# Performance work log

Measured on AMD Instinct MI355X. Metric: run time of the kernel, lower is better.

## Reference

```python
import jax, jax.numpy as jnp
import numpy as np


def _base_index(H, W, dtype=jnp.float32):
    # Homogeneous pixel coordinates (x, y, 1) per pixel, shape [H, W, 3].
    x = jnp.arange(W, dtype=dtype)
    y = jnp.arange(H, dtype=dtype)
    xx, yy = jnp.meshgrid(x, y)  # [H, W]
    return jnp.stack([xx, yy, jnp.ones_like(xx)], axis=-1)


def _bilinear_resample(image, coords):
    # image: [B, H, W, C]; coords: [B, H, W, 2] in (x, y) order (tf resampler convention).
    # Out-of-bounds corners contribute zero (zero padding), matching tfa.image.resampler.
    B, H, W, C = image.shape
    x = coords[..., 0]
    y = coords[..., 1]
    x0 = jnp.floor(x)
    y0 = jnp.floor(y)
    wx1 = x - x0
    wy1 = y - y0
    wx0 = 1.0 - wx1
    wy0 = 1.0 - wy1
    x0i = x0.astype(jnp.int32)
    y0i = y0.astype(jnp.int32)
    x1i = x0i + 1
    y1i = y0i + 1

    def corner(yi, xi, w):
        valid = (xi >= 0) & (xi < W) & (yi >= 0) & (yi < H)
        xc = jnp.clip(xi, 0, W - 1)
        yc = jnp.clip(yi, 0, H - 1)
        # gather per batch: [B, H, W, C]
        g = jax.vmap(lambda im, yy, xx: im[yy, xx])(image, yc, xc)
        return g * (w * valid.astype(image.dtype))[..., None]

    return (corner(y0i, x0i, wy0 * wx0) + corner(y0i, x1i, wy0 * wx1)
            + corner(y1i, x0i, wy1 * wx0) + corner(y1i, x1i, wy1 * wx1))


def setup_inputs() -> dict:
    key = jax.random.key(0)
    k1, k2, k3 = jax.random.split(key, 3)
    B, H, W, C = 4, 512, 640, 16
    image_tensor = jax.random.normal(k1, (B, H, W, C), dtype=jnp.float32)
    # positive depths around 1
    depth_tensor = 0.5 + jax.random.uniform(k2, (B, H, W), dtype=jnp.float32)
    # near-identity projective transform so sampled coords land mostly in-bounds
    eye = jnp.eye(4, dtype=jnp.float32)[None].repeat(B, axis=0)
    project_tensor = eye + 0.001 * jax.random.normal(k3, (B, 4, 4), dtype=jnp.float32)
    return {"image_tensor": image_tensor, "depth_tensor": depth_tensor,
            "project_tensor": project_tensor}


def reference(image_tensor, depth_tensor, project_tensor):
    B, H, W, C = image_tensor.shape
    base = _base_index(H, W, image_tensor.dtype)  # [H, W, 3]
    R = project_tensor[:, :3, :3]                 # [B, 3, 3]
    t = project_tensor[:, :3, 3]                  # [B, 3]
    # tf.tensordot(R, base, [-1,-1]) -> [B,3,H,W]; transpose -> [B,H,W,3]
    rotate = jnp.einsum('bij,hwj->bhwi', R, base)
    sample = rotate * depth_tensor[..., None] + t[:, None, None, :]  # [B,H,W,3]
    coords = sample[..., :2] / sample[..., 2:3]                       # [B,H,W,2] (x,y)
    return _bilinear_resample(image_tensor, coords)
```

## Files before the change

kernel.cpp:

```cpp
#include <hip/hip_runtime.h>

constexpr int B  = 4;
constexpr int H  = 512;
constexpr int Wd = 640;
constexpr int NPIX_IMG = H * Wd;
constexpr int BLOCK = 256;
constexpr int PIX_PER_BLOCK  = BLOCK / 4;
constexpr int BLOCKS_PER_ROW = Wd / PIX_PER_BLOCK;
constexpr int BLOCKS_PER_IMG = H * BLOCKS_PER_ROW;
constexpr int GRID = B * BLOCKS_PER_IMG;
static_assert(Wd % PIX_PER_BLOCK == 0, "block must tile a row exactly");
static_assert(GRID * BLOCK == B * NPIX_IMG * 4, "prefetch exactly covers image");

typedef float f32x4 __attribute__((ext_vector_type(4)));

__global__ __launch_bounds__(256) void depth_project_kernel(
    const float* __restrict__ image,
    const float* __restrict__ depth,
    const float* __restrict__ proj,
    float4* __restrict__ out)
{
    const int blk = blockIdx.x;
    const int tix = threadIdx.x;

    const f32x4* img_v = (const f32x4*)image;
    f32x4 pf = img_v[blk * BLOCK + tix];

    const int b   = blk / BLOCKS_PER_IMG;
    const int rem = blk % BLOCKS_PER_IMG;
    const int h   = rem / BLOCKS_PER_ROW;
    const int wb  = (rem % BLOCKS_PER_ROW) * PIX_PER_BLOCK;

    const int c4  = tix & 3;
    const int pl  = tix >> 2;
    const int w   = wb + pl;
    const int pix = (b * H + h) * Wd + w;

    const float* P = proj + b * 16;
    const float x = (float)w;
    const float y = (float)h;
    const float d = depth[pix];

    float sx = (P[0] * x + P[1] * y + P[2])  * d + P[3];
    float sy = (P[4] * x + P[5] * y + P[6])  * d + P[7];
    float sz = (P[8] * x + P[9] * y + P[10]) * d + P[11];
    float cx = sx / sz;
    float cy = sy / sz;

    float x0f = floorf(cx), y0f = floorf(cy);
    float wx1 = cx - x0f,   wy1 = cy - y0f;
    float wx0 = 1.0f - wx1, wy0 = 1.0f - wy1;
    int x0 = (int)x0f, y0 = (int)y0f;
    int x1 = x0 + 1,   y1 = y0 + 1;

    float vx0 = (x0 >= 0 && x0 < Wd) ? 1.0f : 0.0f;
    float vx1 = (x1 >= 0 && x1 < Wd) ? 1.0f : 0.0f;
    float vy0 = (y0 >= 0 && y0 < H)  ? 1.0f : 0.0f;
    float vy1 = (y1 >= 0 && y1 < H)  ? 1.0f : 0.0f;

    int x0c = min(max(x0, 0), Wd - 1);
    int x1c = min(max(x1, 0), Wd - 1);
    int y0c = min(max(y0, 0), H - 1);
    int y1c = min(max(y1, 0), H - 1);

    float w00 = wy0 * wx0 * vy0 * vx0;
    float w01 = wy0 * wx1 * vy0 * vx1;
    float w10 = wy1 * wx0 * vy1 * vx0;
    float w11 = wy1 * wx1 * vy1 * vx1;

    asm volatile("" :: "v"(pf.x), "v"(pf.y), "v"(pf.z), "v"(pf.w));

    const float4* img4 = (const float4*)image;
    const int base_b = b * (NPIX_IMG * 4);
    float4 g00 = img4[base_b + (y0c * Wd + x0c) * 4 + c4];
    float4 g01 = img4[base_b + (y0c * Wd + x1c) * 4 + c4];
    float4 g10 = img4[base_b + (y1c * Wd + x0c) * 4 + c4];
    float4 g11 = img4[base_b + (y1c * Wd + x1c) * 4 + c4];

    f32x4 r;
    r.x = g00.x * w00 + g01.x * w01 + g10.x * w10 + g11.x * w11;
    r.y = g00.y * w00 + g01.y * w01 + g10.y * w10 + g11.y * w11;
    r.z = g00.z * w00 + g01.z * w01 + g10.z * w10 + g11.z * w11;
    r.w = g00.w * w00 + g01.w * w01 + g10.w * w10 + g11.w * w11;

    f32x4* out_v = (f32x4*)out;
    __builtin_nontemporal_store(r, out_v + pix * 4 + c4);
}

extern "C" void kernel_launch(void* const* d_in, const int* in_sizes, int n_in,
                              void* d_out, int out_size, void* d_ws, size_t ws_size,
                              hipStream_t stream) {
    const float* image = (const float*)d_in[0];
    const float* depth = (const float*)d_in[1];
    const float* proj  = (const float*)d_in[2];
    float4* out = (float4*)d_out;

    depth_project_kernel<<<GRID, BLOCK, 0, stream>>>(image, depth, proj, out);
}
```

Baseline: 155.0 us.

## Stage two source rows in shared memory and gather bilinear corners from LDS

Each block now covers 128 pixels and cooperatively loads a two-row, 144-column window of the source image into a swizzled shared-memory tile. The window is placed using the projected coordinate of the block's middle pixel. Bilinear corners are read from LDS when they fall inside the window and from global memory otherwise. This removes the old whole-image prefetch trick and the redundant global gathers, and depth is now read with a nontemporal load. In exchange it adds two barriers and a serial dependency before any gather can start, and relies on the transform being near identity for the window to hit.

```diff
diff --git a/kernel.cpp b/kernel.cpp
--- a/kernel.cpp
+++ b/kernel.cpp
@@ -4,33 +4,32 @@
 constexpr int H  = 512;
 constexpr int Wd = 640;
 constexpr int NPIX_IMG = H * Wd;
-constexpr int BLOCK = 256;
-constexpr int PIX_PER_BLOCK  = BLOCK / 4;
-constexpr int BLOCKS_PER_ROW = Wd / PIX_PER_BLOCK;
-constexpr int BLOCKS_PER_IMG = H * BLOCKS_PER_ROW;
-constexpr int GRID = B * BLOCKS_PER_IMG;
-static_assert(Wd % PIX_PER_BLOCK == 0, "block must tile a row exactly");
-static_assert(GRID * BLOCK == B * NPIX_IMG * 4, "prefetch exactly covers image");
+constexpr int PXB   = 128;
+constexpr int BLOCK = PXB * 4;
+constexpr int BPR   = Wd / PXB;
+constexpr int GRID  = B * H * BPR;
+constexpr int SW    = 144;
+constexpr int XMARG = PXB / 2 + 7;
+static_assert(Wd % PXB == 0, "block tiles a row exactly");
 
 typedef float f32x4 __attribute__((ext_vector_type(4)));
 
-__global__ __launch_bounds__(256) void depth_project_kernel(
+__global__ __launch_bounds__(BLOCK, 8) void depth_project_kernel(
     const float* __restrict__ image,
     const float* __restrict__ depth,
     const float* __restrict__ proj,
     float4* __restrict__ out)
 {
+    __shared__ float4 tile[2][SW][4];
+    __shared__ int cons[2];
+
     const int blk = blockIdx.x;
+    const int b   = blk / (H * BPR);
+    const int rem = blk % (H * BPR);
+    const int h   = rem / BPR;
+    const int wb  = (rem % BPR) * PXB;
+
     const int tix = threadIdx.x;
-
-    const f32x4* img_v = (const f32x4*)image;
-    f32x4 pf = img_v[blk * BLOCK + tix];
-
-    const int b   = blk / BLOCKS_PER_IMG;
-    const int rem = blk % BLOCKS_PER_IMG;
-    const int h   = rem / BLOCKS_PER_ROW;
-    const int wb  = (rem % BLOCKS_PER_ROW) * PIX_PER_BLOCK;
-
     const int c4  = tix & 3;
     const int pl  = tix >> 2;
     const int w   = wb + pl;
@@ -39,7 +38,7 @@
     const float* P = proj + b * 16;
     const float x = (float)w;
     const float y = (float)h;
-    const float d = depth[pix];
+    const float d = __builtin_nontemporal_load(depth + pix);
 
     float sx = (P[0] * x + P[1] * y + P[2])  * d + P[3];
     float sy = (P[4] * x + P[5] * y + P[6])  * d + P[7];
@@ -52,6 +51,29 @@
     float wx0 = 1.0f - wx1, wy0 = 1.0f - wy1;
     int x0 = (int)x0f, y0 = (int)y0f;
     int x1 = x0 + 1,   y1 = y0 + 1;
+
+    if (tix == BLOCK / 2) {
+        cons[0] = min(max(y0, -8), H + 8);
+        cons[1] = min(max(x0 - XMARG, -2 * SW), Wd + SW);
+    }
+    __syncthreads();
+    const int yhat = cons[0];
+    const int xlo  = cons[1];
+    const int rid0 = min(max(yhat,     0), H - 1);
+    const int rid1 = min(max(yhat + 1, 0), H - 1);
+
+    const float4* img4 = (const float4*)image;
+    const int ibase = b * (NPIX_IMG * 4);
+    for (int e = tix; e < 2 * SW * 4; e += BLOCK) {
+        int r   = (e >= SW * 4) ? 1 : 0;
+        int rm  = e - r * (SW * 4);
+        int col = rm >> 2;
+        int c   = rm & 3;
+        int xc  = min(max(xlo + col, 0), Wd - 1);
+        int rid = r ? rid1 : rid0;
+        tile[r][col][c ^ ((col >> 1) & 3)] = img4[ibase + (rid * Wd + xc) * 4 + c];
+    }
+    __syncthreads();
 
     float vx0 = (x0 >= 0 && x0 < Wd) ? 1.0f : 0.0f;
     float vx1 = (x1 >= 0 && x1 < Wd) ? 1.0f : 0.0f;
@@ -68,14 +90,35 @@
     float w10 = wy1 * wx0 * vy1 * vx0;
     float w11 = wy1 * wx1 * vy1 * vx1;
 
-    asm volatile("" :: "v"(pf.x), "v"(pf.y), "v"(pf.z), "v"(pf.w));
+    const int j0 = x0c - xlo, j1 = x1c - xlo;
+    const bool jok0 = (unsigned)j0 < (unsigned)SW;
+    const bool jok1 = (unsigned)j1 < (unsigned)SW;
+    const int rs0 = (y0c == rid0) ? 0 : ((y0c == rid1) ? 1 : -1);
+    const int rs1 = (y1c == rid0) ? 0 : ((y1c == rid1) ? 1 : -1);
+    const bool h00 = jok0 && (rs0 >= 0);
+    const bool h01 = jok1 && (rs0 >= 0);
+    const bool h10 = jok0 && (rs1 >= 0);
+    const bool h11 = jok1 && (rs1 >= 0);
 
-    const float4* img4 = (const float4*)image;
-    const int base_b = b * (NPIX_IMG * 4);
-    float4 g00 = img4[base_b + (y0c * Wd + x0c) * 4 + c4];
-    float4 g01 = img4[base_b + (y0c * Wd + x1c) * 4 + c4];
-    float4 g10 = img4[base_b + (y1c * Wd + x0c) * 4 + c4];
-    float4 g11 = img4[base_b + (y1c * Wd + x1c) * 4 + c4];
+    const int j0s = min(max(j0, 0), SW - 1);
+    const int j1s = min(max(j1, 0), SW - 1);
+    const int r0s = max(rs0, 0);
+    const int r1s = max(rs1, 0);
+    const int sl0 = c4 ^ ((j0s >> 1) & 3);
+    const int sl1 = c4 ^ ((j1s >> 1) & 3);
+
+    float4 g00 = tile[r0s][j0s][sl0];
+    float4 g01 = tile[r0s][j1s][sl1];
+    float4 g10 = tile[r1s][j0s][sl0];
+    float4 g11 = tile[r1s][j1s][sl1];
+
+    if (!(h00 && h01 && h10 && h11)) {
+        const float4* ib = img4 + ibase;
+        if (!h00) g00 = ib[(y0c * Wd + x0c) * 4 + c4];
+        if (!h01) g01 = ib[(y0c * Wd + x1c) * 4 + c4];
+        if (!h10) g10 = ib[(y1c * Wd + x0c) * 4 + c4];
+        if (!h11) g11 = ib[(y1c * Wd + x1c) * 4 + c4];
+    }
 
     f32x4 r;
     r.x = g00.x * w00 + g01.x * w01 + g10.x * w10 + g11.x * w11;
```

After: 169.0 us. 1.09x slower.

## Process full image rows per block with software-pipelined prefetch and XCD swizzle

Applied to the files above, without the earlier changes.

Each block now handles one whole image row in 64-pixel chunks instead of a single chunk, so the grid shrinks to one block per row. A block index swizzle places consecutive rows on the same XCD so neighbouring gathers can share L2. Depth and an image-prefetch vector for the next chunk are loaded while the current chunk's gathers run. This cuts launch and per-block overhead and improves cache locality, but reduces the number of waves in flight and serialises work inside each block.

```diff
diff --git a/kernel.cpp b/kernel.cpp
--- a/kernel.cpp
+++ b/kernel.cpp
@@ -5,12 +5,12 @@
 constexpr int Wd = 640;
 constexpr int NPIX_IMG = H * Wd;
 constexpr int BLOCK = 256;
-constexpr int PIX_PER_BLOCK  = BLOCK / 4;
-constexpr int BLOCKS_PER_ROW = Wd / PIX_PER_BLOCK;
-constexpr int BLOCKS_PER_IMG = H * BLOCKS_PER_ROW;
-constexpr int GRID = B * BLOCKS_PER_IMG;
-static_assert(Wd % PIX_PER_BLOCK == 0, "block must tile a row exactly");
-static_assert(GRID * BLOCK == B * NPIX_IMG * 4, "prefetch exactly covers image");
+constexpr int ROWS  = B * H;
+constexpr int GRID  = ROWS;
+constexpr int CHUNK = 64;
+constexpr int NCH   = Wd / CHUNK;
+static_assert(NCH * CHUNK == Wd, "chunks tile the row exactly");
+static_assert(ROWS % 8 == 0, "XCD swizzle needs rows % 8 == 0");
 
 typedef float f32x4 __attribute__((ext_vector_type(4)));
 
@@ -23,68 +23,77 @@
     const int blk = blockIdx.x;
     const int tix = threadIdx.x;
 
-    const f32x4* img_v = (const f32x4*)image;
-    f32x4 pf = img_v[blk * BLOCK + tix];
+    const int row = (blk & 7) * (ROWS / 8) + (blk >> 3);
+    const int b   = row / H;
+    const int h   = row % H;
 
-    const int b   = blk / BLOCKS_PER_IMG;
-    const int rem = blk % BLOCKS_PER_IMG;
-    const int h   = rem / BLOCKS_PER_ROW;
-    const int wb  = (rem % BLOCKS_PER_ROW) * PIX_PER_BLOCK;
-
-    const int c4  = tix & 3;
-    const int pl  = tix >> 2;
-    const int w   = wb + pl;
-    const int pix = (b * H + h) * Wd + w;
+    const int c4 = tix & 3;
+    const int pl = tix >> 2;
+    const int rowpix = row * Wd;
 
     const float* P = proj + b * 16;
-    const float x = (float)w;
     const float y = (float)h;
-    const float d = depth[pix];
 
-    float sx = (P[0] * x + P[1] * y + P[2])  * d + P[3];
-    float sy = (P[4] * x + P[5] * y + P[6])  * d + P[7];
-    float sz = (P[8] * x + P[9] * y + P[10]) * d + P[11];
-    float cx = sx / sz;
-    float cy = sy / sz;
+    const f32x4*  img_v = (const f32x4*)image;
+    const float4* img4  = (const float4*)image;
+    const int ibase = b * (NPIX_IMG * 4);
+    f32x4* out_v = (f32x4*)out;
 
-    float x0f = floorf(cx), y0f = floorf(cy);
-    float wx1 = cx - x0f,   wy1 = cy - y0f;
-    float wx0 = 1.0f - wx1, wy0 = 1.0f - wy1;
-    int x0 = (int)x0f, y0 = (int)y0f;
-    int x1 = x0 + 1,   y1 = y0 + 1;
+    float d_cur = depth[rowpix + pl];
+    f32x4 pf = img_v[rowpix * 4 + tix];
 
-    float vx0 = (x0 >= 0 && x0 < Wd) ? 1.0f : 0.0f;
-    float vx1 = (x1 >= 0 && x1 < Wd) ? 1.0f : 0.0f;
-    float vy0 = (y0 >= 0 && y0 < H)  ? 1.0f : 0.0f;
-    float vy1 = (y1 >= 0 && y1 < H)  ? 1.0f : 0.0f;
+    for (int n = 0; n < NCH; ++n) {
+        const int px = n * CHUNK + pl;
+        const float x = (float)px;
 
-    int x0c = min(max(x0, 0), Wd - 1);
-    int x1c = min(max(x1, 0), Wd - 1);
-    int y0c = min(max(y0, 0), H - 1);
-    int y1c = min(max(y1, 0), H - 1);
+        asm volatile("" :: "v"(pf.x), "v"(pf.y), "v"(pf.z), "v"(pf.w));
 
-    float w00 = wy0 * wx0 * vy0 * vx0;
-    float w01 = wy0 * wx1 * vy0 * vx1;
-    float w10 = wy1 * wx0 * vy1 * vx0;
-    float w11 = wy1 * wx1 * vy1 * vx1;
+        float sx = (P[0] * x + P[1] * y + P[2])  * d_cur + P[3];
+        float sy = (P[4] * x + P[5] * y + P[6])  * d_cur + P[7];
+        float sz = (P[8] * x + P[9] * y + P[10]) * d_cur + P[11];
+        float cx = sx / sz;
+        float cy = sy / sz;
 
-    asm volatile("" :: "v"(pf.x), "v"(pf.y), "v"(pf.z), "v"(pf.w));
+        float x0f = floorf(cx), y0f = floorf(cy);
+        float wx1 = cx - x0f,   wy1 = cy - y0f;
+        float wx0 = 1.0f - wx1, wy0 = 1.0f - wy1;
+        int x0 = (int)x0f, y0 = (int)y0f;
+        int x1 = x0 + 1,   y1 = y0 + 1;
 
-    const float4* img4 = (const float4*)image;
-    const int base_b = b * (NPIX_IMG * 4);
-    float4 g00 = img4[base_b + (y0c * Wd + x0c) * 4 + c4];
-    float4 g01 = img4[base_b + (y0c * Wd + x1c) * 4 + c4];
-    float4 g10 = img4[base_b + (y1c * Wd + x0c) * 4 + c4];
-    float4 g11 = img4[base_b + (y1c * Wd + x1c) * 4 + c4];
+        float vx0 = (x0 >= 0 && x0 < Wd) ? 1.0f : 0.0f;
+        float vx1 = (x1 >= 0 && x1 < Wd) ? 1.0f : 0.0f;
+        float vy0 = (y0 >= 0 && y0 < H)  ? 1.0f : 0.0f;
+        float vy1 = (y1 >= 0 && y1 < H)  ? 1.0f : 0.0f;
 
-    f32x4 r;
-    r.x = g00.x * w00 + g01.x * w01 + g10.x * w10 + g11.x * w11;
-    r.y = g00.y * w00 + g01.y * w01 + g10.y * w10 + g11.y * w11;
-    r.z = g00.z * w00 + g01.z * w01 + g10.z * w10 + g11.z * w11;
-    r.w = g00.w * w00 + g01.w * w01 + g10.w * w10 + g11.w * w11;
+        int x0c = min(max(x0, 0), Wd - 1);
+        int x1c = min(max(x1, 0), Wd - 1);
+        int y0c = min(max(y0, 0), H - 1);
+        int y1c = min(max(y1, 0), H - 1);
 
-    f32x4* out_v = (f32x4*)out;
-    __builtin_nontemporal_store(r, out_v + pix * 4 + c4);
+        float w00 = wy0 * wx0 * vy0 * vx0;
+        float w01 = wy0 * wx1 * vy0 * vx1;
+        float w10 = wy1 * wx0 * vy1 * vx0;
+        float w11 = wy1 * wx1 * vy1 * vx1;
+
+        float4 g00 = img4[ibase + (y0c * Wd + x0c) * 4 + c4];
+        float4 g01 = img4[ibase + (y0c * Wd + x1c) * 4 + c4];
+        float4 g10 = img4[ibase + (y1c * Wd + x0c) * 4 + c4];
+        float4 g11 = img4[ibase + (y1c * Wd + x1c) * 4 + c4];
+
+        const int nn = (n + 1 < NCH) ? n + 1 : NCH - 1;
+        pf = img_v[(rowpix + nn * CHUNK) * 4 + tix];
+        float d_next = depth[rowpix + nn * CHUNK + pl];
+
+        f32x4 r;
+        r.x = g00.x * w00 + g01.x * w01 + g10.x * w10 + g11.x * w11;
+        r.y = g00.y * w00 + g01.y * w01 + g10.y * w10 + g11.y * w11;
+        r.z = g00.z * w00 + g01.z * w01 + g10.z * w10 + g11.z * w11;
+        r.w = g00.w * w00 + g01.w * w01 + g10.w * w10 + g11.w * w11;
+
+        __builtin_nontemporal_store(r, out_v + (rowpix + px) * 4 + c4);
+
+        d_cur = d_next;
+    }
 }
 
 extern "C" void kernel_launch(void* const* d_in, const int* in_sizes, int n_in,
```

Result: slower. 167.4 us (+8.0%).

## Stage predicted source rows in an LDS ring buffer for bilinear gathers

Applied to the files above, without the earlier changes.

Each block now processes a 128-pixel strip over 16 output rows. It predicts which source rows the projected coordinates will hit and keeps a 4-row ring of image data with a 32-column margin in shared memory. Gathers read from LDS and fall back to global memory when a sample lands outside the staged window. Upcoming rows are prefetched into registers while the current row is computed. This aims to turn scattered global gathers into coalesced row loads that are reused across pixels. In exchange it adds two barriers per step, far less parallelism (about 1/32 as many blocks), and the removal of the old whole-image prefetch trick.

```diff
diff --git a/kernel.cpp b/kernel.cpp
--- a/kernel.cpp
+++ b/kernel.cpp
@@ -4,13 +4,17 @@
 constexpr int H  = 512;
 constexpr int Wd = 640;
 constexpr int NPIX_IMG = H * Wd;
-constexpr int BLOCK = 256;
-constexpr int PIX_PER_BLOCK  = BLOCK / 4;
-constexpr int BLOCKS_PER_ROW = Wd / PIX_PER_BLOCK;
-constexpr int BLOCKS_PER_IMG = H * BLOCKS_PER_ROW;
-constexpr int GRID = B * BLOCKS_PER_IMG;
-static_assert(Wd % PIX_PER_BLOCK == 0, "block must tile a row exactly");
-static_assert(GRID * BLOCK == B * NPIX_IMG * 4, "prefetch exactly covers image");
+constexpr int BLOCK  = 256;
+constexpr int STRIP  = 128;
+constexpr int NSTEP  = 16;
+constexpr int STRIPS = Wd / STRIP;
+constexpr int LAYERS = H / NSTEP;
+constexpr int GRID   = B * LAYERS * STRIPS;
+constexpr int XM     = 32;
+constexpr int SW     = 192;
+constexpr int SEGF4  = SW * 4;
+constexpr int RING   = 4;
+static_assert(STRIPS * STRIP == Wd && LAYERS * NSTEP == H, "exact tiling");
 
 typedef float f32x4 __attribute__((ext_vector_type(4)));
 
@@ -20,71 +24,148 @@
     const float* __restrict__ proj,
     float4* __restrict__ out)
 {
-    const int blk = blockIdx.x;
+    __shared__ f32x4 tile[RING * SEGF4];
+
+    const int blk   = blockIdx.x;
+    const int b     = blk / (LAYERS * STRIPS);
+    const int r2    = blk % (LAYERS * STRIPS);
+    const int layer = r2 / STRIPS;
+    const int strip = r2 % STRIPS;
+    const int h0    = layer * NSTEP;
+    const int wb    = strip * STRIP;
+    const int xlo   = wb - XM;
+
     const int tix = threadIdx.x;
-
-    const f32x4* img_v = (const f32x4*)image;
-    f32x4 pf = img_v[blk * BLOCK + tix];
-
-    const int b   = blk / BLOCKS_PER_IMG;
-    const int rem = blk % BLOCKS_PER_IMG;
-    const int h   = rem / BLOCKS_PER_ROW;
-    const int wb  = (rem % BLOCKS_PER_ROW) * PIX_PER_BLOCK;
-
     const int c4  = tix & 3;
     const int pl  = tix >> 2;
-    const int w   = wb + pl;
-    const int pix = (b * H + h) * Wd + w;
 
     const float* P = proj + b * 16;
-    const float x = (float)w;
-    const float y = (float)h;
-    const float d = depth[pix];
+    const float p0=P[0],p1=P[1],p2=P[2],p3=P[3],p4=P[4],p5=P[5],
+                p6=P[6],p7=P[7],p8=P[8],p9=P[9],p10=P[10],p11=P[11];
 
-    float sx = (P[0] * x + P[1] * y + P[2])  * d + P[3];
-    float sy = (P[4] * x + P[5] * y + P[6])  * d + P[7];
-    float sz = (P[8] * x + P[9] * y + P[10]) * d + P[11];
-    float cx = sx / sz;
-    float cy = sy / sz;
+    const f32x4* imgv = (const f32x4*)image;
+    const int ibase = b * (NPIX_IMG * 4);
+    f32x4* out_v = (f32x4*)out;
 
-    float x0f = floorf(cx), y0f = floorf(cy);
-    float wx1 = cx - x0f,   wy1 = cy - y0f;
-    float wx0 = 1.0f - wx1, wy0 = 1.0f - wy1;
-    int x0 = (int)x0f, y0 = (int)y0f;
-    int x1 = x0 + 1,   y1 = y0 + 1;
+    auto predict = [&](int hh) -> int {
+        const float xc = (float)(wb + 64), yc = (float)hh;
+        float sy = (p4 * xc + p5 * yc + p6) + p7;
+        float sz = (p8 * xc + p9 * yc + p10) + p11;
+        float cy = sy / sz;
+        cy = fminf(fmaxf(cy, -1.0e6f), 1.0e6f);
+        return (int)floorf(cy) - 1;
+    };
 
-    float vx0 = (x0 >= 0 && x0 < Wd) ? 1.0f : 0.0f;
-    float vx1 = (x1 >= 0 && x1 < Wd) ? 1.0f : 0.0f;
-    float vy0 = (y0 >= 0 && y0 < H)  ? 1.0f : 0.0f;
-    float vy1 = (y1 >= 0 && y1 < H)  ? 1.0f : 0.0f;
+    auto load_row = [&](int r, f32x4& a, f32x4& c, f32x4& e) {
+        const int rc = min(max(r, 0), H - 1);
+        const int rb = ibase + rc * (Wd * 4);
+        {   int idx = tix;       int col = idx >> 2, cc = idx & 3;
+            int xc = min(max(xlo + col, 0), Wd - 1);
+            a = imgv[rb + xc * 4 + cc]; }
+        {   int idx = tix + 256; int col = idx >> 2, cc = idx & 3;
+            int xc = min(max(xlo + col, 0), Wd - 1);
+            c = imgv[rb + xc * 4 + cc]; }
+        {   int idx = tix + 512; int col = idx >> 2, cc = idx & 3;
+            int xc = min(max(xlo + col, 0), Wd - 1);
+            e = imgv[rb + xc * 4 + cc]; }
+    };
+    auto write_row = [&](int r, const f32x4& a, const f32x4& c, const f32x4& e) {
+        const int slot = r & 3;
+        tile[slot * SEGF4 + tix]       = a;
+        tile[slot * SEGF4 + tix + 256] = c;
+        tile[slot * SEGF4 + tix + 512] = e;
+    };
 
-    int x0c = min(max(x0, 0), Wd - 1);
-    int x1c = min(max(x1, 0), Wd - 1);
-    int y0c = min(max(y0, 0), H - 1);
-    int y1c = min(max(y1, 0), H - 1);
+    int lo_cur = min(max(predict(h0), -4), H);
+    f32x4 rA0,rA1,rA2, rB0,rB1,rB2, rC0,rC1,rC2, rD0,rD1,rD2;
+    load_row(lo_cur + 0, rA0, rA1, rA2);
+    load_row(lo_cur + 1, rB0, rB1, rB2);
+    load_row(lo_cur + 2, rC0, rC1, rC2);
+    load_row(lo_cur + 3, rD0, rD1, rD2);
+    float d0 = depth[(b * H + h0) * Wd + wb + pl];
+    float d1 = depth[(b * H + h0) * Wd + wb + 64 + pl];
+    write_row(lo_cur + 0, rA0, rA1, rA2);
+    write_row(lo_cur + 1, rB0, rB1, rB2);
+    write_row(lo_cur + 2, rC0, rC1, rC2);
+    write_row(lo_cur + 3, rD0, rD1, rD2);
+    __syncthreads();
 
-    float w00 = wy0 * wx0 * vy0 * vx0;
-    float w01 = wy0 * wx1 * vy0 * vx1;
-    float w10 = wy1 * wx0 * vy1 * vx0;
-    float w11 = wy1 * wx1 * vy1 * vx1;
+    f32x4 pA0,pA1,pA2, pB0,pB1,pB2;
 
-    asm volatile("" :: "v"(pf.x), "v"(pf.y), "v"(pf.z), "v"(pf.w));
+    for (int s = 0; s < NSTEP; ++s) {
+        const int lo_next = min(max(predict(h0 + s + 1), lo_cur), lo_cur + 2);
+        const int npend = lo_next - lo_cur;
 
-    const float4* img4 = (const float4*)image;
-    const int base_b = b * (NPIX_IMG * 4);
-    float4 g00 = img4[base_b + (y0c * Wd + x0c) * 4 + c4];
-    float4 g01 = img4[base_b + (y0c * Wd + x1c) * 4 + c4];
-    float4 g10 = img4[base_b + (y1c * Wd + x0c) * 4 + c4];
-    float4 g11 = img4[base_b + (y1c * Wd + x1c) * 4 + c4];
+        if (npend >= 1) load_row(lo_cur + 4, pA0, pA1, pA2);
+        if (npend >= 2) load_row(lo_cur + 5, pB0, pB1, pB2);
+        const int hn = h0 + min(s + 1, NSTEP - 1);
+        const float dn0 = depth[(b * H + hn) * Wd + wb + pl];
+        const float dn1 = depth[(b * H + hn) * Wd + wb + 64 + pl];
 
-    f32x4 r;
-    r.x = g00.x * w00 + g01.x * w01 + g10.x * w10 + g11.x * w11;
-    r.y = g00.y * w00 + g01.y * w01 + g10.y * w10 + g11.y * w11;
-    r.z = g00.z * w00 + g01.z * w01 + g10.z * w10 + g11.z * w11;
-    r.w = g00.w * w00 + g01.w * w01 + g10.w * w10 + g11.w * w11;
+        const float y = (float)(h0 + s);
+#pragma unroll
+        for (int k = 0; k < 2; ++k) {
+            const int   px = wb + (k << 6) + pl;
+            const float dd = k ? d1 : d0;
+            const float x  = (float)px;
 
-    f32x4* out_v = (f32x4*)out;
-    __builtin_nontemporal_store(r, out_v + pix * 4 + c4);
+            float sx = (p0 * x + p1 * y + p2)  * dd + p3;
+            float sy = (p4 * x + p5 * y + p6)  * dd + p7;
+            float sz = (p8 * x + p9 * y + p10) * dd + p11;
+            float cx = sx / sz, cy = sy / sz;
+
+            float x0f = floorf(cx), y0f = floorf(cy);
+            float wx1 = cx - x0f,   wy1 = cy - y0f;
+            float wx0 = 1.0f - wx1, wy0 = 1.0f - wy1;
+            int x0 = (int)x0f, y0 = (int)y0f;
+            int x1 = x0 + 1,   y1 = y0 + 1;
+
+            float vx0 = (x0 >= 0 && x0 < Wd) ? 1.0f : 0.0f;
+            float vx1 = (x1 >= 0 && x1 < Wd) ? 1.0f : 0.0f;
+            float vy0 = (y0 >= 0 && y0 < H)  ? 1.0f : 0.0f;
+            float vy1 = (y1 >= 0 && y1 < H)  ? 1.0f : 0.0f;
+
+            int x0c = min(max(x0, 0), Wd - 1), x1c = min(max(x1, 0), Wd - 1);
+            int y0c = min(max(y0, 0), H - 1),  y1c = min(max(y1, 0), H - 1);
+
+            float w00 = wy0 * wx0 * vy0 * vx0, w01 = wy0 * wx1 * vy0 * vx1;
+            float w10 = wy1 * wx0 * vy1 * vx0, w11 = wy1 * wx1 * vy1 * vx1;
+
+            const int j0 = x0c - xlo, j1 = x1c - xlo;
+            const bool jok0 = (unsigned)j0 < (unsigned)SW;
+            const bool jok1 = (unsigned)j1 < (unsigned)SW;
+            const bool rok0 = (unsigned)(y0c - lo_cur) < (unsigned)RING;
+            const bool rok1 = (unsigned)(y1c - lo_cur) < (unsigned)RING;
+            const int s0 = y0c & 3, s1 = y1c & 3;
+            const int j0s = jok0 ? j0 : 0, j1s = jok1 ? j1 : 0;
+
+            f32x4 g00 = tile[s0 * SEGF4 + j0s * 4 + c4];
+            f32x4 g01 = tile[s0 * SEGF4 + j1s * 4 + c4];
+            f32x4 g10 = tile[s1 * SEGF4 + j0s * 4 + c4];
+            f32x4 g11 = tile[s1 * SEGF4 + j1s * 4 + c4];
+
+            const bool c00 = rok0 && jok0, c01 = rok0 && jok1;
+            const bool c10 = rok1 && jok0, c11 = rok1 && jok1;
+            if (!(c00 && c01 && c10 && c11)) {
+                const f32x4* ib = imgv + ibase;
+                if (!c00) g00 = ib[(y0c * Wd + x0c) * 4 + c4];
+                if (!c01) g01 = ib[(y0c * Wd + x1c) * 4 + c4];
+                if (!c10) g10 = ib[(y1c * Wd + x0c) * 4 + c4];
+                if (!c11) g11 = ib[(y1c * Wd + x1c) * 4 + c4];
+            }
+
+            f32x4 r = g00 * w00 + g01 * w01 + g10 * w10 + g11 * w11;
+            __builtin_nontemporal_store(r, out_v + ((b * H + h0 + s) * Wd + px) * 4 + c4);
+        }
+
+        __syncthreads();
+        if (npend >= 1) write_row(lo_cur + 4, pA0, pA1, pA2);
+        if (npend >= 2) write_row(lo_cur + 5, pB0, pB1, pB2);
+        __syncthreads();
+
+        lo_cur = lo_next;
+        d0 = dn0; d1 = dn1;
+    }
 }
 
 extern "C" void kernel_launch(void* const* d_in, const int* in_sizes, int n_in,
```

After: 186.5 us. 20.3% more time.
